# Kernel optimization log

Measured on AMD Instinct MI355X. Metric: run time of the kernel, lower is better.

Reference implementation:

```python
import jax, jax.numpy as jnp
import numpy as np

N_NODES = 100000


def _gcn_conv(h, src, dst, norm, b, num_nodes):
    # h: [N, D] already linearly transformed; aggregate norm-weighted messages at dst
    msgs = norm[:, None] * h[src]                      # [E+N, D] gather
    out = jax.ops.segment_sum(msgs, dst, num_segments=num_nodes)  # scatter-add
    return out + b


def _norm_and_loops(edge_index, num_nodes):
    # add self-loops and compute symmetric degree normalization (GCNConv default)
    loop = jnp.arange(num_nodes, dtype=edge_index.dtype)
    src = jnp.concatenate([edge_index[0], loop])
    dst = jnp.concatenate([edge_index[1], loop])
    deg = jax.ops.segment_sum(jnp.ones_like(dst, dtype=jnp.float32), dst,
                              num_segments=num_nodes)
    dinv = jnp.where(deg > 0, jax.lax.rsqrt(jnp.maximum(deg, 1.0)), 0.0)
    norm = dinv[src] * dinv[dst]
    return src, dst, norm


def setup_inputs() -> dict:
    key = jax.random.key(0)
    k1, k2, k3, k4 = jax.random.split(key, 4)
    x = jax.random.normal(k1, (N_NODES, 512), dtype=jnp.float32)
    edge_index = jax.random.randint(k2, (2, 3200000), 0, N_NODES, dtype=jnp.int64)
    W1 = jax.random.normal(k3, (512, 16), dtype=jnp.float32) * (1.0 / np.sqrt(512))
    b1 = jnp.zeros((16,), dtype=jnp.float32)
    W2 = jax.random.normal(k4, (16, 7), dtype=jnp.float32) * (1.0 / np.sqrt(16))
    b2 = jnp.zeros((7,), dtype=jnp.float32)
    return {"x": x, "edge_index": edge_index, "W1": W1, "b1": b1, "W2": W2, "b2": b2}


def reference(x, edge_index, W1, b1, W2, b2):
    n = x.shape[0]
    src, dst, norm = _norm_and_loops(edge_index, n)
    h = _gcn_conv(x @ W1, src, dst, norm, b1, n)   # layer 1
    h = jax.nn.relu(h)                              # dropout off in eval mode
    h = _gcn_conv(h @ W2, src, dst, norm, b2, n)   # layer 2
    return jax.nn.log_softmax(h, axis=1)
```

## Files before the change

kernel.cpp:

```cpp
#include <hip/hip_runtime.h>
#include <hip/hip_bf16.h>


#define N_NODES 100000
#define NPAD    100352
#define D_IN    512
#define H1DIM   16
#define C_PAD   8
#define NB      196
#define NBUCK   512
#define BCAP    8192
#define TILE_A  8192


__global__ __launch_bounds__(256) void k_initcur(int* __restrict__ cursor) {
    int i = blockIdx.x * 256 + threadIdx.x;
    if (i < NBUCK) cursor[i] = i * BCAP;
}

__global__ __launch_bounds__(512) void k_passA(const int* __restrict__ src,
                                               const int* __restrict__ dst, int E,
                                               int* __restrict__ cursor,
                                               unsigned* __restrict__ packed) {
    __shared__ int hist[NBUCK];
    __shared__ int wp[NBUCK];
    int tile0 = blockIdx.x * TILE_A;
    for (int i = threadIdx.x; i < NBUCK; i += 512) hist[i] = 0;
    __syncthreads();
    unsigned pay[16];
    unsigned short bk[16];
#pragma unroll
    for (int r = 0; r < 16; ++r) {
        int e = tile0 + r * 512 + threadIdx.x;
        if (e < E) {
            unsigned d = (unsigned)dst[e];
            unsigned s = (unsigned)src[e];
            unsigned b = d / NB;
            pay[r] = ((d - b * NB) << 17) | s;
            bk[r] = (unsigned short)b;
            atomicAdd(&hist[b], 1);
        } else {
            bk[r] = 0xffffu;
        }
    }
    __syncthreads();
    {
        int c = hist[threadIdx.x];
        wp[threadIdx.x] = c ? atomicAdd(&cursor[threadIdx.x], c) : 0;
    }
    __syncthreads();
#pragma unroll
    for (int r = 0; r < 16; ++r) {
        if (bk[r] != 0xffffu) {
            int pos = atomicAdd(&wp[bk[r]], 1);
            int lim = ((int)bk[r] + 1) * BCAP;
            if (pos < lim) packed[pos] = pay[r];
        }
    }
}

__global__ __launch_bounds__(256) void k_passB(const unsigned* __restrict__ packed,
                                               const int* __restrict__ cursor,
                                               int* __restrict__ sorted_src,
                                               int* __restrict__ offs,
                                               int* __restrict__ cnt_out,
                                               float* __restrict__ dinv) {
    __shared__ unsigned ent[BCAP];
    __shared__ int sorted[BCAP];
    __shared__ int hist[NB + 1];
    __shared__ int scan[NB + 1];
    __shared__ int wp[NB];
    int b = blockIdx.x;
    int base = b * BCAP;
    int cnt = cursor[b] - base;
    if (cnt > BCAP) cnt = BCAP;
    for (int i = threadIdx.x; i < cnt; i += 256) ent[i] = packed[base + i];
    for (int i = threadIdx.x; i <= NB; i += 256) hist[i] = 0;
    __syncthreads();
    for (int i = threadIdx.x; i < cnt; i += 256) atomicAdd(&hist[ent[i] >> 17], 1);
    __syncthreads();
    if (threadIdx.x <= NB)
        scan[threadIdx.x] = (threadIdx.x == 0) ? 0 : hist[threadIdx.x - 1];
    __syncthreads();
    for (int off = 1; off < 256; off <<= 1) {
        int v = 0;
        if (threadIdx.x <= NB && threadIdx.x >= off) v = scan[threadIdx.x - off];
        __syncthreads();
        if (threadIdx.x <= NB) scan[threadIdx.x] += v;
        __syncthreads();
    }
    int node0 = b * NB;
    if (threadIdx.x < NB) {
        int node = node0 + threadIdx.x;
        if (node < N_NODES) {
            int h = hist[threadIdx.x];
            cnt_out[node] = h;
            offs[node] = base + scan[threadIdx.x];
            dinv[node] = rsqrtf(1.0f + (float)h);
        }
        wp[threadIdx.x] = scan[threadIdx.x];
    }
    __syncthreads();
    for (int i = threadIdx.x; i < cnt; i += 256) {
        unsigned p = ent[i];
        int pos = atomicAdd(&wp[p >> 17], 1);
        sorted[pos] = (int)(p & 0x1FFFFu);
    }
    __syncthreads();
    for (int i = threadIdx.x; i < cnt; i += 256) sorted_src[base + i] = sorted[i];
}


__global__ __launch_bounds__(256) void k_gemm1(const float* __restrict__ x,
                                               const float4* __restrict__ W14,
                                               float* __restrict__ h1) {
    __shared__ float4 Wl[2048];
    for (int g = threadIdx.x; g < 2048; g += 256) {
        int d = g >> 2, q = g & 3;
        Wl[d * 4 + ((q + (d >> 2)) & 3)] = W14[g];
    }
    int row = blockIdx.x * 64 + (threadIdx.x >> 2);
    int sub = threadIdx.x & 3;
    __syncthreads();
    if (row >= N_NODES) return;
    const float4* xr = (const float4*)(x + (size_t)row * D_IN);
    float acc[16];
#pragma unroll
    for (int k = 0; k < 16; ++k) acc[k] = 0.0f;

#pragma unroll 2
    for (int i = 0; i < 32; ++i) {
        int d4 = sub + i * 4;
        float4 xv = xr[d4];
        int rot = d4 & 3;
#pragma unroll
        for (int r = 0; r < 4; ++r) {
            int d = d4 * 4 + r;
            float xs = (r == 0) ? xv.x : (r == 1) ? xv.y : (r == 2) ? xv.z : xv.w;
#pragma unroll
            for (int q = 0; q < 4; ++q) {
                float4 wv = Wl[d * 4 + ((q + rot) & 3)];
                acc[q * 4 + 0] = fmaf(xs, wv.x, acc[q * 4 + 0]);
                acc[q * 4 + 1] = fmaf(xs, wv.y, acc[q * 4 + 1]);
                acc[q * 4 + 2] = fmaf(xs, wv.z, acc[q * 4 + 2]);
                acc[q * 4 + 3] = fmaf(xs, wv.w, acc[q * 4 + 3]);
            }
        }
    }
#pragma unroll
    for (int k = 0; k < 16; ++k) {
        acc[k] += __shfl_xor(acc[k], 1);
        acc[k] += __shfl_xor(acc[k], 2);
    }
    float4 o;
    if (sub == 0)      o = make_float4(acc[0],  acc[1],  acc[2],  acc[3]);
    else if (sub == 1) o = make_float4(acc[4],  acc[5],  acc[6],  acc[7]);
    else if (sub == 2) o = make_float4(acc[8],  acc[9],  acc[10], acc[11]);
    else               o = make_float4(acc[12], acc[13], acc[14], acc[15]);
    ((float4*)(h1 + (size_t)row * H1DIM))[sub] = o;
}

__global__ __launch_bounds__(256) void k_msg1g2(const int* __restrict__ offs,
                                                const int* __restrict__ cnt_,
                                                const int* __restrict__ ssrc,
                                                const float* __restrict__ dinv,
                                                const float* __restrict__ h1,
                                                const float* __restrict__ b1,
                                                const float* __restrict__ W2,
                                                float* __restrict__ h2) {
    int node = blockIdx.x * 4 + (threadIdx.x >> 6);
    if (node >= N_NODES) return;
    int lane = threadIdx.x & 63;
    int s = lane >> 4;
    int k = lane & 15;
    int off = offs[node];
    int cnt = cnt_[node];
    float acc = 0.0f;
    for (int c = s; c < cnt; c += 4) {
        int sv = ssrc[off + c];
        acc = fmaf(dinv[sv], h1[(size_t)sv * H1DIM + k], acc);
    }
    acc += __shfl_xor(acc, 16);
    acc += __shfl_xor(acc, 32);
    float di = dinv[node];
    float v = fmaf(di, acc, fmaf(di * di, h1[(size_t)node * H1DIM + k], b1[k]));
    v = fmaxf(v, 0.0f);
    int j = lane & 7, kh = lane >> 3;
    float t1 = __shfl(v, kh);
    float t2 = __shfl(v, kh + 8);
    float w1 = (j < 7) ? W2[kh * 7 + j] : 0.0f;
    float w2 = (j < 7) ? W2[(kh + 8) * 7 + j] : 0.0f;
    float p = t1 * w1 + t2 * w2;
    p += __shfl_xor(p, 8);
    p += __shfl_xor(p, 16);
    p += __shfl_xor(p, 32);
    if (lane < 8) h2[(size_t)node * C_PAD + j] = (j < 7) ? p : 0.0f;
}

__global__ __launch_bounds__(256) void k_msg2sm(const int* __restrict__ offs,
                                                const int* __restrict__ cnt_,
                                                const int* __restrict__ ssrc,
                                                const float* __restrict__ dinv,
                                                const float* __restrict__ h2,
                                                const float* __restrict__ b2,
                                                float* __restrict__ out) {
    int node = blockIdx.x * 4 + (threadIdx.x >> 6);
    if (node >= N_NODES) return;
    int lane = threadIdx.x & 63;
    int s = lane >> 3;
    int j = lane & 7;
    int off = offs[node];
    int cnt = cnt_[node];
    float acc = 0.0f;
    for (int c = s; c < cnt; c += 8) {
        int sv = ssrc[off + c];
        acc = fmaf(dinv[sv], h2[(size_t)sv * C_PAD + j], acc);
    }
    acc += __shfl_xor(acc, 8);
    acc += __shfl_xor(acc, 16);
    acc += __shfl_xor(acc, 32);
    float di = dinv[node];
    float v = (j < 7)
        ? fmaf(di, acc, fmaf(di * di, h2[(size_t)node * C_PAD + j], b2[j]))
        : -INFINITY;
    float m = v;
    m = fmaxf(m, __shfl_xor(m, 1));
    m = fmaxf(m, __shfl_xor(m, 2));
    m = fmaxf(m, __shfl_xor(m, 4));
    float e = expf(v - m);
    float ss = e;
    ss += __shfl_xor(ss, 1);
    ss += __shfl_xor(ss, 2);
    ss += __shfl_xor(ss, 4);
    float r = v - m - logf(ss);
    if (s == 0 && j < 7) out[(size_t)node * 7 + j] = r;
}


extern "C" void kernel_launch(void* const* d_in, const int* in_sizes, int n_in,
                              void* d_out, int out_size, void* d_ws, size_t ws_size,
                              hipStream_t stream) {
    const float* x  = (const float*)d_in[0];
    const int*   ei = (const int*)d_in[1];
    const float* W1 = (const float*)d_in[2];
    const float* b1 = (const float*)d_in[3];
    const float* W2 = (const float*)d_in[4];
    const float* b2 = (const float*)d_in[5];
    float* out = (float*)d_out;

    const int E = in_sizes[1] / 2;
    const int* src = ei;
    const int* dst = ei + E;

    char* w = (char*)d_ws;
    size_t off = 0;
    auto alloc = [&](size_t bytes) -> void* {
        off = (off + 255) & ~(size_t)255;
        void* p = w + off;
        off += bytes;
        return p;
    };
    int*      cursor     = (int*)alloc(NBUCK * 4);
    int*      count      = (int*)alloc(NPAD * 4);
    int*      offs       = (int*)alloc(NPAD * 4);
    float*    dinv       = (float*)alloc(NPAD * 4);
    unsigned* packed     = (unsigned*)alloc((size_t)NBUCK * BCAP * 4);
    int*      sorted_src = (int*)alloc((size_t)NBUCK * BCAP * 4);
    float*    h1         = (float*)alloc((size_t)N_NODES * H1DIM * 4);
    float*    h2         = (float*)alloc((size_t)N_NODES * C_PAD * 4);
    (void)ws_size;

    const int gA = (E + TILE_A - 1) / TILE_A;
    const int gN4 = (N_NODES + 3) / 4;

    k_initcur<<<(NBUCK + 255) / 256, 256, 0, stream>>>(cursor);
    k_passA<<<gA, 512, 0, stream>>>(src, dst, E, cursor, packed);
    k_passB<<<NBUCK, 256, 0, stream>>>(packed, cursor, sorted_src, offs, count, dinv);

    k_gemm1<<<(N_NODES + 63) / 64, 256, 0, stream>>>(x, (const float4*)W1, h1);
    k_msg1g2<<<gN4, 256, 0, stream>>>(offs, count, sorted_src, dinv, h1, b1, W2, h2);
    k_msg2sm<<<gN4, 256, 0, stream>>>(offs, count, sorted_src, dinv, h2, b2, out);
}
```

Measured before the change: 496.4 us.

## Prescale features by dinv and vectorize padded CSR neighbor index loads

The source-side degree normalization is folded into the producer kernels, so h1 and h2 are stored already multiplied by dinv. This removes the per-edge dinv gather in both aggregation kernels. Each node's CSR segment in passB is padded to a multiple of 4 with zeroed slots, so the aggregation loops can load neighbor indices as int4 and issue four feature gathers per iteration. The cost is slightly more sorted_src space and writes, plus masking of the padded tail entries. Bucket overflow risk also rises because padding inflates usage against BCAP.

```diff
diff --git a/kernel.cpp b/kernel.cpp
--- a/kernel.cpp
+++ b/kernel.cpp
@@ -68,25 +68,26 @@
     __shared__ unsigned ent[BCAP];
     __shared__ int sorted[BCAP];
     __shared__ int hist[NB + 1];
-    __shared__ int scan[NB + 1];
+    __shared__ int scanA[NB + 1];
     __shared__ int wp[NB];
     int b = blockIdx.x;
     int base = b * BCAP;
     int cnt = cursor[b] - base;
     if (cnt > BCAP) cnt = BCAP;
     for (int i = threadIdx.x; i < cnt; i += 256) ent[i] = packed[base + i];
+    for (int i = threadIdx.x; i < BCAP; i += 256) sorted[i] = 0;
     for (int i = threadIdx.x; i <= NB; i += 256) hist[i] = 0;
     __syncthreads();
     for (int i = threadIdx.x; i < cnt; i += 256) atomicAdd(&hist[ent[i] >> 17], 1);
     __syncthreads();
     if (threadIdx.x <= NB)
-        scan[threadIdx.x] = (threadIdx.x == 0) ? 0 : hist[threadIdx.x - 1];
+        scanA[threadIdx.x] = (threadIdx.x == 0) ? 0 : ((hist[threadIdx.x - 1] + 3) & ~3);
     __syncthreads();
     for (int off = 1; off < 256; off <<= 1) {
         int v = 0;
-        if (threadIdx.x <= NB && threadIdx.x >= off) v = scan[threadIdx.x - off];
+        if (threadIdx.x <= NB && threadIdx.x >= off) v = scanA[threadIdx.x - off];
         __syncthreads();
-        if (threadIdx.x <= NB) scan[threadIdx.x] += v;
+        if (threadIdx.x <= NB) scanA[threadIdx.x] += v;
         __syncthreads();
     }
     int node0 = b * NB;
@@ -95,10 +96,10 @@
         if (node < N_NODES) {
             int h = hist[threadIdx.x];
             cnt_out[node] = h;
-            offs[node] = base + scan[threadIdx.x];
+            offs[node] = base + scanA[threadIdx.x];
             dinv[node] = rsqrtf(1.0f + (float)h);
         }
-        wp[threadIdx.x] = scan[threadIdx.x];
+        wp[threadIdx.x] = scanA[threadIdx.x];
     }
     __syncthreads();
     for (int i = threadIdx.x; i < cnt; i += 256) {
@@ -107,13 +108,15 @@
         sorted[pos] = (int)(p & 0x1FFFFu);
     }
     __syncthreads();
-    for (int i = threadIdx.x; i < cnt; i += 256) sorted_src[base + i] = sorted[i];
+    int totA = scanA[NB];
+    for (int i = threadIdx.x; i < totA; i += 256) sorted_src[base + i] = sorted[i];
 }
 
 
 __global__ __launch_bounds__(256) void k_gemm1(const float* __restrict__ x,
                                                const float4* __restrict__ W14,
-                                               float* __restrict__ h1) {
+                                               const float* __restrict__ dinv,
+                                               float* __restrict__ h1s) {
     __shared__ float4 Wl[2048];
     for (int g = threadIdx.x; g < 2048; g += 256) {
         int d = g >> 2, q = g & 3;
@@ -152,22 +155,24 @@
         acc[k] += __shfl_xor(acc[k], 1);
         acc[k] += __shfl_xor(acc[k], 2);
     }
+    float di = dinv[row];
     float4 o;
     if (sub == 0)      o = make_float4(acc[0],  acc[1],  acc[2],  acc[3]);
     else if (sub == 1) o = make_float4(acc[4],  acc[5],  acc[6],  acc[7]);
     else if (sub == 2) o = make_float4(acc[8],  acc[9],  acc[10], acc[11]);
     else               o = make_float4(acc[12], acc[13], acc[14], acc[15]);
-    ((float4*)(h1 + (size_t)row * H1DIM))[sub] = o;
+    o.x *= di; o.y *= di; o.z *= di; o.w *= di;
+    ((float4*)(h1s + (size_t)row * H1DIM))[sub] = o;
 }
 
 __global__ __launch_bounds__(256) void k_msg1g2(const int* __restrict__ offs,
                                                 const int* __restrict__ cnt_,
                                                 const int* __restrict__ ssrc,
                                                 const float* __restrict__ dinv,
-                                                const float* __restrict__ h1,
+                                                const float* __restrict__ h1s,
                                                 const float* __restrict__ b1,
                                                 const float* __restrict__ W2,
-                                                float* __restrict__ h2) {
+                                                float* __restrict__ h2s) {
     int node = blockIdx.x * 4 + (threadIdx.x >> 6);
     if (node >= N_NODES) return;
     int lane = threadIdx.x & 63;
@@ -176,14 +181,21 @@
     int off = offs[node];
     int cnt = cnt_[node];
     float acc = 0.0f;
-    for (int c = s; c < cnt; c += 4) {
-        int sv = ssrc[off + c];
-        acc = fmaf(dinv[sv], h1[(size_t)sv * H1DIM + k], acc);
+    for (int c0 = s * 4; c0 < cnt; c0 += 16) {
+        int4 sv = *(const int4*)(ssrc + off + c0);
+        float g0 = h1s[(size_t)(unsigned)sv.x * H1DIM + k];
+        float g1 = h1s[(size_t)(unsigned)sv.y * H1DIM + k];
+        float g2 = h1s[(size_t)(unsigned)sv.z * H1DIM + k];
+        float g3 = h1s[(size_t)(unsigned)sv.w * H1DIM + k];
+        acc += g0;
+        acc += (c0 + 1 < cnt) ? g1 : 0.0f;
+        acc += (c0 + 2 < cnt) ? g2 : 0.0f;
+        acc += (c0 + 3 < cnt) ? g3 : 0.0f;
     }
     acc += __shfl_xor(acc, 16);
     acc += __shfl_xor(acc, 32);
     float di = dinv[node];
-    float v = fmaf(di, acc, fmaf(di * di, h1[(size_t)node * H1DIM + k], b1[k]));
+    float v = fmaf(di, acc + h1s[(size_t)node * H1DIM + k], b1[k]);
     v = fmaxf(v, 0.0f);
     int j = lane & 7, kh = lane >> 3;
     float t1 = __shfl(v, kh);
@@ -194,14 +206,14 @@
     p += __shfl_xor(p, 8);
     p += __shfl_xor(p, 16);
     p += __shfl_xor(p, 32);
-    if (lane < 8) h2[(size_t)node * C_PAD + j] = (j < 7) ? p : 0.0f;
+    if (lane < 8) h2s[(size_t)node * C_PAD + j] = (j < 7) ? di * p : 0.0f;
 }
 
 __global__ __launch_bounds__(256) void k_msg2sm(const int* __restrict__ offs,
                                                 const int* __restrict__ cnt_,
                                                 const int* __restrict__ ssrc,
                                                 const float* __restrict__ dinv,
-                                                const float* __restrict__ h2,
+                                                const float* __restrict__ h2s,
                                                 const float* __restrict__ b2,
                                                 float* __restrict__ out) {
     int node = blockIdx.x * 4 + (threadIdx.x >> 6);
@@ -212,16 +224,23 @@
     int off = offs[node];
     int cnt = cnt_[node];
     float acc = 0.0f;
-    for (int c = s; c < cnt; c += 8) {
-        int sv = ssrc[off + c];
-        acc = fmaf(dinv[sv], h2[(size_t)sv * C_PAD + j], acc);
+    for (int c0 = s * 4; c0 < cnt; c0 += 32) {
+        int4 sv = *(const int4*)(ssrc + off + c0);
+        float g0 = h2s[(size_t)(unsigned)sv.x * C_PAD + j];
+        float g1 = h2s[(size_t)(unsigned)sv.y * C_PAD + j];
+        float g2 = h2s[(size_t)(unsigned)sv.z * C_PAD + j];
+        float g3 = h2s[(size_t)(unsigned)sv.w * C_PAD + j];
+        acc += g0;
+        acc += (c0 + 1 < cnt) ? g1 : 0.0f;
+        acc += (c0 + 2 < cnt) ? g2 : 0.0f;
+        acc += (c0 + 3 < cnt) ? g3 : 0.0f;
     }
     acc += __shfl_xor(acc, 8);
     acc += __shfl_xor(acc, 16);
     acc += __shfl_xor(acc, 32);
     float di = dinv[node];
     float v = (j < 7)
-        ? fmaf(di, acc, fmaf(di * di, h2[(size_t)node * C_PAD + j], b2[j]))
+        ? fmaf(di, acc + h2s[(size_t)node * C_PAD + j], b2[j])
         : -INFINITY;
     float m = v;
     m = fmaxf(m, __shfl_xor(m, 1));
@@ -264,10 +283,10 @@
     int*      count      = (int*)alloc(NPAD * 4);
     int*      offs       = (int*)alloc(NPAD * 4);
     float*    dinv       = (float*)alloc(NPAD * 4);
+    float*    h2s        = (float*)alloc((size_t)N_NODES * C_PAD * 4);
+    float*    h1s        = (float*)alloc((size_t)N_NODES * H1DIM * 4);
     unsigned* packed     = (unsigned*)alloc((size_t)NBUCK * BCAP * 4);
     int*      sorted_src = (int*)alloc((size_t)NBUCK * BCAP * 4);
-    float*    h1         = (float*)alloc((size_t)N_NODES * H1DIM * 4);
-    float*    h2         = (float*)alloc((size_t)N_NODES * C_PAD * 4);
     (void)ws_size;
 
     const int gA = (E + TILE_A - 1) / TILE_A;
@@ -277,7 +296,7 @@
     k_passA<<<gA, 512, 0, stream>>>(src, dst, E, cursor, packed);
     k_passB<<<NBUCK, 256, 0, stream>>>(packed, cursor, sorted_src, offs, count, dinv);
 
-    k_gemm1<<<(N_NODES + 63) / 64, 256, 0, stream>>>(x, (const float4*)W1, h1);
-    k_msg1g2<<<gN4, 256, 0, stream>>>(offs, count, sorted_src, dinv, h1, b1, W2, h2);
-    k_msg2sm<<<gN4, 256, 0, stream>>>(offs, count, sorted_src, dinv, h2, b2, out);
-}
+    k_gemm1<<<(N_NODES + 63) / 64, 256, 0, stream>>>(x, (const float4*)W1, dinv, h1s);
+    k_msg1g2<<<gN4, 256, 0, stream>>>(offs, count, sorted_src, dinv, h1s, b1, W2, h2s);
+    k_msg2sm<<<gN4, 256, 0, stream>>>(offs, count, sorted_src, dinv, h2s, b2, out);
+}
```

Measured after the change: 440.1 us. 11.3% less time.
